# Performance work log

Hardware: AMD Instinct MI355X
Metric: run time of the kernel (lower is better)

## Reference

```python
import jax, jax.numpy as jnp
import numpy as np

MAX_SHIFT = 15
EPS = 1e-8


def setup_inputs() -> dict:
    key = jax.random.key(0)
    k1, k2 = jax.random.split(key)
    B, T = 2048, 2048
    preds = jax.random.normal(k1, (B, T), dtype=jnp.float32)
    targets = jax.random.normal(k2, (B, T), dtype=jnp.float32)
    return {"preds": preds, "targets": targets}


def reference(preds, targets):
    # targets statistics (shared across shifts)
    tc = targets - jnp.mean(targets, axis=1, keepdims=True)          # [B, T]
    std_t = jnp.sqrt(jnp.sum(tc * tc, axis=1) + EPS)                 # [B]

    shifts = jnp.arange(-MAX_SHIFT, MAX_SHIFT + 1)                   # [S]

    def pearson_for_shift(s):
        ps = jnp.roll(preds, s, axis=1)                              # [B, T]
        pc = ps - jnp.mean(ps, axis=1, keepdims=True)
        std_p = jnp.sqrt(jnp.sum(pc * pc, axis=1) + EPS)             # [B]
        cov = jnp.sum(pc * tc, axis=1)                               # [B]
        return cov / (std_p * std_t)

    pearsons = jax.vmap(pearson_for_shift)(shifts)                   # [S, B]
    best = jnp.maximum(jnp.max(pearsons, axis=0), -1.0)              # [B], init -1
    return 1.0 - jnp.mean(best)
```

## Files before the change

### kernel.cpp

```cpp
#include <hip/hip_runtime.h>

#define TLEN 2048
#define BROWS 2048
#define NSHIFT 31
#define MAXSH 15
#define BLOCK 256
#define EPSF 1e-8f

__device__ __forceinline__ int padidx12(int k) { return 12 * (k >> 3) + (k & 7); }

template<int CTRL, int RMASK, bool BC>
__device__ __forceinline__ float dpp_mov(float v, float old) {
    return __int_as_float(__builtin_amdgcn_update_dpp(
        __float_as_int(old), __float_as_int(v), CTRL, RMASK, 0xF, BC));
}
__device__ __forceinline__ float wave_sum_dpp(float v) {
    v += dpp_mov<0x111, 0xF, true>(v, 0.f);
    v += dpp_mov<0x112, 0xF, true>(v, 0.f);
    v += dpp_mov<0x114, 0xF, true>(v, 0.f);
    v += dpp_mov<0x118, 0xF, true>(v, 0.f);
    v += dpp_mov<0x142, 0xA, true>(v, 0.f);
    v += dpp_mov<0x143, 0xC, true>(v, 0.f);
    return v;
}
__device__ __forceinline__ float wave_max_dpp(float v) {
    v = fmaxf(v, dpp_mov<0x111, 0xF, false>(v, v));
    v = fmaxf(v, dpp_mov<0x112, 0xF, false>(v, v));
    v = fmaxf(v, dpp_mov<0x114, 0xF, false>(v, v));
    v = fmaxf(v, dpp_mov<0x118, 0xF, false>(v, v));
    v = fmaxf(v, dpp_mov<0x142, 0xA, false>(v, v));
    v = fmaxf(v, dpp_mov<0x143, 0xC, false>(v, v));
    return v;
}

__global__ void __launch_bounds__(BLOCK, 4)
pearson_rows_kernel(const float* __restrict__ preds,
                    const float* __restrict__ targets,
                    float* __restrict__ row_best)
{
    __shared__ float smem[3392];
    float* wsum = smem + 3120;
    float* rbuf = smem + 3376;

    const int tid  = threadIdx.x;
    const int wave = tid >> 6;
    const int lane = tid & 63;
    const int row  = blockIdx.x;
    const float* p_row = preds   + (size_t)row * TLEN;
    const float* t_row = targets + (size_t)row * TLEN;

    float pc[8];
    {
        float4 a = ((const float4*)p_row)[2 * tid];
        float4 b = ((const float4*)p_row)[2 * tid + 1];
        pc[0] = a.x; pc[1] = a.y; pc[2] = a.z; pc[3] = a.w;
        pc[4] = b.x; pc[5] = b.y; pc[6] = b.z; pc[7] = b.w;
    }
    float sp = 0.f, spp = 0.f;
    #pragma unroll
    for (int i = 0; i < 8; ++i) { sp += pc[i]; spp = fmaf(pc[i], pc[i], spp); }

    float st = 0.f, stt = 0.f;
    #pragma unroll
    for (int r = 0; r < 2; ++r) {
        int f4 = tid + r * BLOCK;
        float4 tv = ((const float4*)t_row)[f4];
        st  += tv.x + tv.y + tv.z + tv.w;
        stt = fmaf(tv.x, tv.x, stt); stt = fmaf(tv.y, tv.y, stt);
        stt = fmaf(tv.z, tv.z, stt); stt = fmaf(tv.w, tv.w, stt);
        int k = f4 * 4 + MAXSH;
        smem[padidx12(k)]     = tv.x;
        smem[padidx12(k + 1)] = tv.y;
        smem[padidx12(k + 2)] = tv.z;
        smem[padidx12(k + 3)] = tv.w;
    }
    if (tid < MAXSH) {
        smem[padidx12(tid)] = t_row[TLEN - MAXSH + tid];
    } else if (tid >= 32 && tid < 32 + MAXSH) {
        int i = tid - 32;
        smem[padidx12(TLEN + MAXSH + i)] = t_row[i];
    }

    sp  = wave_sum_dpp(sp);
    spp = wave_sum_dpp(spp);
    st  = wave_sum_dpp(st);
    stt = wave_sum_dpp(stt);
    if (lane == 63) {
        *(float4*)(rbuf + wave * 4) = make_float4(sp, spp, st, stt);
    }
    __syncthreads();

    float w[38];
    {
        const float* g = smem + 12 * tid;
        #pragma unroll
        for (int q = 0; q < 4; ++q) {
            float4 a = *(const float4*)(g + 12 * q);
            float4 b = *(const float4*)(g + 12 * q + 4);
            w[8*q + 0] = a.x; w[8*q + 1] = a.y; w[8*q + 2] = a.z; w[8*q + 3] = a.w;
            w[8*q + 4] = b.x; w[8*q + 5] = b.y; w[8*q + 6] = b.z; w[8*q + 7] = b.w;
        }
        float4 c = *(const float4*)(g + 48);
        float2 e = *(const float2*)(g + 52);
        w[32] = c.x; w[33] = c.y; w[34] = c.z; w[35] = c.w;
        w[36] = e.x; w[37] = e.y;
        #pragma unroll
        for (int d = 0; d < 38; ++d) asm volatile("" : "+v"(w[d]));
    }

    float acc[NSHIFT];
    #pragma unroll
    for (int s = 0; s < NSHIFT; ++s) acc[s] = 0.f;
    #pragma unroll
    for (int m = 0; m < 8; ++m) {
        #pragma unroll
        for (int s = 0; s < NSHIFT; ++s) acc[s] = fmaf(pc[m], w[m + s], acc[s]);
    }

    #pragma unroll
    for (int s = 0; s < NSHIFT; ++s) acc[s] = wave_sum_dpp(acc[s]);
    if (lane == 63) {
        float* dst = wsum + wave * 64;
        *(float4*)(dst +  0) = make_float4(acc[0],  acc[1],  acc[2],  acc[3]);
        *(float4*)(dst +  4) = make_float4(acc[4],  acc[5],  acc[6],  acc[7]);
        *(float4*)(dst +  8) = make_float4(acc[8],  acc[9],  acc[10], acc[11]);
        *(float4*)(dst + 12) = make_float4(acc[12], acc[13], acc[14], acc[15]);
        *(float4*)(dst + 16) = make_float4(acc[16], acc[17], acc[18], acc[19]);
        *(float4*)(dst + 20) = make_float4(acc[20], acc[21], acc[22], acc[23]);
        *(float4*)(dst + 24) = make_float4(acc[24], acc[25], acc[26], acc[27]);
        *(float2*)(dst + 28) = make_float2(acc[28], acc[29]);
        dst[30] = acc[30];
    }
    __syncthreads();

    if (wave == 0) {
        float dot = wsum[lane] + wsum[64 + lane] + wsum[128 + lane] + wsum[192 + lane];
        float4 r0 = *(const float4*)(rbuf + 0);
        float4 r1 = *(const float4*)(rbuf + 4);
        float4 r2 = *(const float4*)(rbuf + 8);
        float4 r3 = *(const float4*)(rbuf + 12);
        float SP  = r0.x + r1.x + r2.x + r3.x;
        float SPP = r0.y + r1.y + r2.y + r3.y;
        float ST  = r0.z + r1.z + r2.z + r3.z;
        float STT = r0.w + r1.w + r2.w + r3.w;
        const float invT = 1.0f / TLEN;
        float mp = SP * invT, mt = ST * invT;
        float varp = SPP - (float)TLEN * mp * mp;
        float vart = STT - (float)TLEN * mt * mt;
        float corr = (float)TLEN * mp * mt;
        float pear = (dot - corr) * rsqrtf((varp + EPSF) * (vart + EPSF));
        float v = (lane < NSHIFT) ? pear : -3.0e38f;
        v = wave_max_dpp(v);
        if (lane == 63) row_best[row] = fmaxf(v, -1.0f);
    }
}

__global__ void __launch_bounds__(BLOCK)
pearson_finalize_kernel(const float* __restrict__ row_best, float* __restrict__ out)
{
    __shared__ float r[4];
    const int tid = threadIdx.x, wave = tid >> 6, lane = tid & 63;
    float4 a = ((const float4*)row_best)[tid];
    float4 b = ((const float4*)row_best)[tid + BLOCK];
    float s = (a.x + a.y) + (a.z + a.w) + (b.x + b.y) + (b.z + b.w);
    s = wave_sum_dpp(s);
    if (lane == 63) r[wave] = s;
    __syncthreads();
    if (tid == 0)
        out[0] = 1.0f - (r[0] + r[1] + r[2] + r[3]) * (1.0f / (float)BROWS);
}

extern "C" void kernel_launch(void* const* d_in, const int* in_sizes, int n_in,
                              void* d_out, int out_size, void* d_ws, size_t ws_size,
                              hipStream_t stream) {
    const float* preds   = (const float*)d_in[0];
    const float* targets = (const float*)d_in[1];
    float* row_best = (float*)d_ws;
    float* out      = (float*)d_out;
    pearson_rows_kernel<<<BROWS, BLOCK, 0, stream>>>(preds, targets, row_best);
    pearson_finalize_kernel<<<1, BLOCK, 0, stream>>>(row_best, out);
}
```

Measured before the change: 80.99 us.

## Replace per-shift wave reductions with transpose-style permlane swap reduction tree

```diff
diff --git a/kernel.cpp b/kernel.cpp
--- a/kernel.cpp
+++ b/kernel.cpp
@@ -32,15 +32,51 @@
     v = fmaxf(v, dpp_mov<0x143, 0xC, false>(v, v));
     return v;
 }
+__device__ __forceinline__ float row16_sum(float v) {
+    v += dpp_mov<0x128, 0xF, true>(v, 0.f);
+    v += dpp_mov<0x124, 0xF, true>(v, 0.f);
+    v += dpp_mov<0x122, 0xF, true>(v, 0.f);
+    v += dpp_mov<0x121, 0xF, true>(v, 0.f);
+    return v;
+}
+
+#if __has_builtin(__builtin_amdgcn_permlane32_swap)
+__device__ __forceinline__ float pswap32_add(float x, float y) {
+    auto r = __builtin_amdgcn_permlane32_swap(
+        __float_as_uint(x), __float_as_uint(y), false, false);
+    return __uint_as_float(r[0]) + __uint_as_float(r[1]);
+}
+#else
+__device__ __forceinline__ float pswap32_add(float x, float y) {
+    bool hi = (threadIdx.x & 32) != 0;
+    float keep = hi ? y : x;
+    float send = hi ? x : y;
+    return keep + __shfl_xor(send, 32, 64);
+}
+#endif
+#if __has_builtin(__builtin_amdgcn_permlane16_swap)
+__device__ __forceinline__ float pswap16_add(float x, float y) {
+    auto r = __builtin_amdgcn_permlane16_swap(
+        __float_as_uint(x), __float_as_uint(y), false, false);
+    return __uint_as_float(r[0]) + __uint_as_float(r[1]);
+}
+#else
+__device__ __forceinline__ float pswap16_add(float x, float y) {
+    bool hi = (threadIdx.x & 16) != 0;
+    float keep = hi ? y : x;
+    float send = hi ? x : y;
+    return keep + __shfl_xor(send, 16, 64);
+}
+#endif
 
 __global__ void __launch_bounds__(BLOCK, 4)
 pearson_rows_kernel(const float* __restrict__ preds,
                     const float* __restrict__ targets,
                     float* __restrict__ row_best)
 {
-    __shared__ float smem[3392];
+    __shared__ float smem[3264];
     float* wsum = smem + 3120;
-    float* rbuf = smem + 3376;
+    float* rbuf = smem + 3248;
 
     const int tid  = threadIdx.x;
     const int wave = tid >> 6;
@@ -108,33 +144,40 @@
         for (int d = 0; d < 38; ++d) asm volatile("" : "+v"(w[d]));
     }
 
-    float acc[NSHIFT];
-    #pragma unroll
-    for (int s = 0; s < NSHIFT; ++s) acc[s] = 0.f;
-    #pragma unroll
-    for (int m = 0; m < 8; ++m) {
+    float acc[32];
+    #pragma unroll
+    for (int s = 0; s < NSHIFT; ++s) acc[s] = pc[0] * w[s];
+    #pragma unroll
+    for (int m = 1; m < 8; ++m) {
         #pragma unroll
         for (int s = 0; s < NSHIFT; ++s) acc[s] = fmaf(pc[m], w[m + s], acc[s]);
     }
-
-    #pragma unroll
-    for (int s = 0; s < NSHIFT; ++s) acc[s] = wave_sum_dpp(acc[s]);
-    if (lane == 63) {
-        float* dst = wsum + wave * 64;
-        *(float4*)(dst +  0) = make_float4(acc[0],  acc[1],  acc[2],  acc[3]);
-        *(float4*)(dst +  4) = make_float4(acc[4],  acc[5],  acc[6],  acc[7]);
-        *(float4*)(dst +  8) = make_float4(acc[8],  acc[9],  acc[10], acc[11]);
-        *(float4*)(dst + 12) = make_float4(acc[12], acc[13], acc[14], acc[15]);
-        *(float4*)(dst + 16) = make_float4(acc[16], acc[17], acc[18], acc[19]);
-        *(float4*)(dst + 20) = make_float4(acc[20], acc[21], acc[22], acc[23]);
-        *(float4*)(dst + 24) = make_float4(acc[24], acc[25], acc[26], acc[27]);
-        *(float2*)(dst + 28) = make_float2(acc[28], acc[29]);
-        dst[30] = acc[30];
+    acc[31] = acc[30];
+
+    float r16[16];
+    #pragma unroll
+    for (int i = 0; i < 16; ++i) r16[i] = pswap32_add(acc[i], acc[i + 16]);
+    float q[8];
+    #pragma unroll
+    for (int i = 0; i < 8; ++i) q[i] = pswap16_add(r16[i], r16[i + 8]);
+    #pragma unroll
+    for (int i = 0; i < 8; ++i) q[i] = row16_sum(q[i]);
+
+    {
+        float s01 = (lane & 1) ? q[1] : q[0];
+        float s23 = (lane & 1) ? q[3] : q[2];
+        float s45 = (lane & 1) ? q[5] : q[4];
+        float s67 = (lane & 1) ? q[7] : q[6];
+        float s03 = (lane & 2) ? s23 : s01;
+        float s47 = (lane & 2) ? s67 : s45;
+        float sel = (lane & 4) ? s47 : s03;
+        if (!(lane & 8)) wsum[wave * 32 + (lane & 7) + 8 * (lane >> 4)] = sel;
     }
     __syncthreads();
 
     if (wave == 0) {
-        float dot = wsum[lane] + wsum[64 + lane] + wsum[128 + lane] + wsum[192 + lane];
+        int slot = lane & 31;
+        float dot = wsum[slot] + wsum[32 + slot] + wsum[64 + slot] + wsum[96 + slot];
         float4 r0 = *(const float4*)(rbuf + 0);
         float4 r1 = *(const float4*)(rbuf + 4);
         float4 r2 = *(const float4*)(rbuf + 8);
@@ -149,8 +192,7 @@
         float vart = STT - (float)TLEN * mt * mt;
         float corr = (float)TLEN * mp * mt;
         float pear = (dot - corr) * rsqrtf((varp + EPSF) * (vart + EPSF));
-        float v = (lane < NSHIFT) ? pear : -3.0e38f;
-        v = wave_max_dpp(v);
+        float v = wave_max_dpp(pear);
         if (lane == 63) row_best[row] = fmaxf(v, -1.0f);
     }
 }
```

New measurement: 78.37 us, median of 2. 3.2% less time.
